# Performance work log

Measured on AMD Instinct MI355X. Metric: run time of the kernel, lower is better.

The kernel has to match this reference:

```python
import jax, jax.numpy as jnp
import numpy as np

N = 16384
F_IN = 64
F_OUT = 64


def setup_inputs() -> dict:
    key = jax.random.key(0)
    k1, k2, k3 = jax.random.split(key, 3)
    x = jax.random.normal(k1, (N, F_IN), dtype=jnp.float32)
    # dense binary adjacency (what dense_to_sparse consumes)
    adj = jax.random.randint(k2, (N, N), 0, 2).astype(jnp.float32)
    W = jax.random.normal(k3, (F_IN, F_OUT), dtype=jnp.float32) * (1.0 / np.sqrt(F_IN))
    b = jnp.zeros((F_OUT,), dtype=jnp.float32)
    return {"x": x, "adj": adj, "W": W, "b": b}


def reference(x, adj, W, b):
    # GCNConv with edge_weight from dense_to_sparse(adj), add_self_loops=True,
    # symmetric normalization: out = D^{-1/2} A_hat^T D^{-1/2} (x W) + b,
    # where A_hat = adj + I and D is the column-degree of A_hat.
    # Dropout is identity in eval mode (training=False). Activation = relu.
    deg = adj.sum(axis=0) + 1.0                      # [N] col sums incl. self-loop
    dinv = jnp.where(deg > 0, jax.lax.rsqrt(deg), 0.0)
    xw = x @ W                                       # [N, F_OUT]
    z = dinv[:, None] * xw                           # scale by source deg^-1/2
    # A_hat^T @ z = adj^T @ z + z (self-loop term), avoids materializing A + I
    out = dinv[:, None] * (adj.T @ z + z) + b
    return jax.nn.relu(out)
```

## Files before the change

kernel.cpp:

```cpp
#include <hip/hip_runtime.h>
#include <cstdint>
#include <cstddef>

#define GN 16384
#define GF 64
#define NW (GN / 32)

typedef __bf16 bf16x8 __attribute__((ext_vector_type(8)));
typedef float f32x4 __attribute__((ext_vector_type(4)));
typedef unsigned int u32x4 __attribute__((ext_vector_type(4)));

__device__ __forceinline__ bf16x8 decode8(unsigned int b) {
  unsigned int t = (b & 0xffu) * 0x8001u;
  u32x4 r;
  r[0] = (t & 0x00010001u) * 0x3F80u;
  r[1] = ((t >> 2) & 0x00010001u) * 0x3F80u;
  r[2] = ((t >> 4) & 0x00010001u) * 0x3F80u;
  r[3] = ((t >> 6) & 0x00010001u) * 0x3F80u;
  return __builtin_bit_cast(bf16x8, r);
}

__device__ __forceinline__ unsigned short f2bf(float v) {
  unsigned int u = __builtin_bit_cast(unsigned int, v);
  u += 0x7fffu + ((u >> 16) & 1u);
  return (unsigned short)(u >> 16);
}

__device__ __forceinline__ float bf2f(unsigned short s) {
  return __builtin_bit_cast(float, (unsigned int)s << 16);
}

__global__ __launch_bounds__(256) void k_pack(const float* __restrict__ adj,
                                              float* __restrict__ deg,
                                              unsigned int* __restrict__ packed) {
  const int cb = blockIdx.x >> 5;
  const int jb = blockIdx.x & 31;
  const int col0 = cb * 1024 + threadIdx.x * 4;
  const int j0 = jb * 512;
  int cnt0 = 0, cnt1 = 0, cnt2 = 0, cnt3 = 0;

  u32x4 vv0[4], vv1[4], vv2[4], vv3[4];

#pragma unroll
  for (int seg = 0; seg < 4; ++seg) {
#pragma unroll
    for (int q = 0; q < 4; ++q) {
      unsigned int w0 = 0, w1 = 0, w2 = 0, w3 = 0;
      const float* base = adj + (size_t)(j0 + seg * 128 + q * 32) * GN + col0;
#pragma unroll 8
      for (int b = 0; b < 32; ++b) {
        f32x4 a = *(const f32x4*)(base + (size_t)b * GN);
        unsigned int m = 1u << b;
        if (a.x != 0.f) w0 |= m;
        if (a.y != 0.f) w1 |= m;
        if (a.z != 0.f) w2 |= m;
        if (a.w != 0.f) w3 |= m;
      }
      vv0[seg][q] = w0; vv1[seg][q] = w1; vv2[seg][q] = w2; vv3[seg][q] = w3;
      cnt0 += __popc(w0); cnt1 += __popc(w1); cnt2 += __popc(w2); cnt3 += __popc(w3);
    }
  }
  unsigned int* p0 = packed + (size_t)(col0 + 0) * NW + (size_t)jb * 16;
  unsigned int* p1 = packed + (size_t)(col0 + 1) * NW + (size_t)jb * 16;
  unsigned int* p2 = packed + (size_t)(col0 + 2) * NW + (size_t)jb * 16;
  unsigned int* p3 = packed + (size_t)(col0 + 3) * NW + (size_t)jb * 16;
#pragma unroll
  for (int seg = 0; seg < 4; ++seg) *(u32x4*)(p0 + seg * 4) = vv0[seg];
#pragma unroll
  for (int seg = 0; seg < 4; ++seg) *(u32x4*)(p1 + seg * 4) = vv1[seg];
#pragma unroll
  for (int seg = 0; seg < 4; ++seg) *(u32x4*)(p2 + seg * 4) = vv2[seg];
#pragma unroll
  for (int seg = 0; seg < 4; ++seg) *(u32x4*)(p3 + seg * 4) = vv3[seg];

  atomicAdd(&deg[col0 + 0], (float)cnt0);
  atomicAdd(&deg[col0 + 1], (float)cnt1);
  atomicAdd(&deg[col0 + 2], (float)cnt2);
  atomicAdd(&deg[col0 + 3], (float)cnt3);
}

__global__ __launch_bounds__(256) void k_z(const float* __restrict__ x,
                                           const float* __restrict__ W,
                                           const float* __restrict__ deg,
                                           float* __restrict__ dinv,
                                           unsigned short* __restrict__ z_rm,
                                           unsigned short* __restrict__ z2) {
  __shared__ float Wl[64][64];
  __shared__ float xl[64][64];
  const int tid = threadIdx.x;
  const int f = tid & 63;
  const int w = tid >> 6;
  const int rowB = blockIdx.x * 64;

  for (int idx = tid; idx < 4096; idx += 256) {
    Wl[idx >> 6][idx & 63] = W[idx];
    xl[idx >> 6][idx & 63] = x[(size_t)rowB * 64 + idx];
  }
  __syncthreads();

  float acc[16];
#pragma unroll
  for (int r = 0; r < 16; ++r) acc[r] = 0.f;
  for (int k = 0; k < 64; ++k) {
    float wk = Wl[k][f];
#pragma unroll
    for (int r = 0; r < 16; ++r) acc[r] = fmaf(xl[w * 16 + r][k], wk, acc[r]);
  }

  const int row0 = rowB + w * 16;
  if (f < 16) {
    int row = row0 + f;
    dinv[row] = 1.0f / sqrtf(deg[row] + 1.0f);
  }

  unsigned short zs[16];
#pragma unroll
  for (int r = 0; r < 16; ++r) {
    int row = row0 + r;
    float di = 1.0f / sqrtf(deg[row] + 1.0f);
    unsigned short zb = f2bf(di * acc[r]);
    zs[r] = zb;
    z_rm[(size_t)row * GF + f] = zb;
  }
  unsigned int p[8];
#pragma unroll
  for (int i = 0; i < 8; ++i)
    p[i] = (unsigned int)zs[2 * i] | ((unsigned int)zs[2 * i + 1] << 16);
  char* dst = (char*)z2 + (size_t)((rowB >> 5) + (w >> 1)) * 4096 + f * 64 + (w & 1) * 32;
  u32x4 lo = {p[0], p[1], p[2], p[3]};
  u32x4 hi = {p[4], p[5], p[6], p[7]};
  *(u32x4*)dst = lo;
  *(u32x4*)(dst + 16) = hi;
}

__global__ __launch_bounds__(512) void k_spmm(const unsigned int* __restrict__ packed,
                                              const unsigned short* __restrict__ z2,
                                              const unsigned short* __restrict__ z_rm,
                                              const float* __restrict__ dinv,
                                              const float* __restrict__ bias,
                                              float* __restrict__ out) {
  __shared__ float red[4][64][64];
  const int i0 = blockIdx.x * 64;
  const int tid = threadIdx.x;
  const int wid = tid >> 6, lane = tid & 63;
  const int lrow = lane & 15, kb = lane >> 4;
  const int sh = kb * 8;

  f32x4 acc[4][4];
#pragma unroll
  for (int m = 0; m < 4; ++m)
#pragma unroll
    for (int n = 0; n < 4; ++n) acc[m][n] = (f32x4){0.f, 0.f, 0.f, 0.f};

  const unsigned int* pr0 = packed + (size_t)(i0 + 0 * 16 + lrow) * NW + wid * 64;
  const unsigned int* pr1 = packed + (size_t)(i0 + 1 * 16 + lrow) * NW + wid * 64;
  const unsigned int* pr2 = packed + (size_t)(i0 + 2 * 16 + lrow) * NW + wid * 64;
  const unsigned int* pr3 = packed + (size_t)(i0 + 3 * 16 + lrow) * NW + wid * 64;
  const char* zbase = (const char*)z2 + (size_t)(wid * 64) * 4096 + lrow * 64 + kb * 16;

  bf16x8 cur0 = *(const bf16x8*)(zbase + 0 * 1024);
  bf16x8 cur1 = *(const bf16x8*)(zbase + 1 * 1024);
  bf16x8 cur2 = *(const bf16x8*)(zbase + 2 * 1024);
  bf16x8 cur3 = *(const bf16x8*)(zbase + 3 * 1024);
  u32x4 bits0 = *(const u32x4*)pr0;
  u32x4 bits1 = *(const u32x4*)pr1;
  u32x4 bits2 = *(const u32x4*)pr2;
  u32x4 bits3 = *(const u32x4*)pr3;

  for (int it = 0; it < 16; ++it) {
    u32x4 nb0 = *(const u32x4*)(pr0 + 4);
    u32x4 nb1 = *(const u32x4*)(pr1 + 4);
    u32x4 nb2 = *(const u32x4*)(pr2 + 4);
    u32x4 nb3 = *(const u32x4*)(pr3 + 4);
#pragma unroll
    for (int s = 0; s < 4; ++s) {
      const char* zn = zbase + (s + 1) * 4096;
      bf16x8 n0 = *(const bf16x8*)(zn + 0 * 1024);
      bf16x8 n1 = *(const bf16x8*)(zn + 1 * 1024);
      bf16x8 n2 = *(const bf16x8*)(zn + 2 * 1024);
      bf16x8 n3 = *(const bf16x8*)(zn + 3 * 1024);

      bf16x8 a0 = decode8(bits0[s] >> sh);
      acc[0][0] = __builtin_amdgcn_mfma_f32_16x16x32_bf16(a0, cur0, acc[0][0], 0, 0, 0);
      acc[0][1] = __builtin_amdgcn_mfma_f32_16x16x32_bf16(a0, cur1, acc[0][1], 0, 0, 0);
      acc[0][2] = __builtin_amdgcn_mfma_f32_16x16x32_bf16(a0, cur2, acc[0][2], 0, 0, 0);
      acc[0][3] = __builtin_amdgcn_mfma_f32_16x16x32_bf16(a0, cur3, acc[0][3], 0, 0, 0);
      bf16x8 a1 = decode8(bits1[s] >> sh);
      acc[1][0] = __builtin_amdgcn_mfma_f32_16x16x32_bf16(a1, cur0, acc[1][0], 0, 0, 0);
      acc[1][1] = __builtin_amdgcn_mfma_f32_16x16x32_bf16(a1, cur1, acc[1][1], 0, 0, 0);
      acc[1][2] = __builtin_amdgcn_mfma_f32_16x16x32_bf16(a1, cur2, acc[1][2], 0, 0, 0);
      acc[1][3] = __builtin_amdgcn_mfma_f32_16x16x32_bf16(a1, cur3, acc[1][3], 0, 0, 0);
      bf16x8 a2 = decode8(bits2[s] >> sh);
      acc[2][0] = __builtin_amdgcn_mfma_f32_16x16x32_bf16(a2, cur0, acc[2][0], 0, 0, 0);
      acc[2][1] = __builtin_amdgcn_mfma_f32_16x16x32_bf16(a2, cur1, acc[2][1], 0, 0, 0);
      acc[2][2] = __builtin_amdgcn_mfma_f32_16x16x32_bf16(a2, cur2, acc[2][2], 0, 0, 0);
      acc[2][3] = __builtin_amdgcn_mfma_f32_16x16x32_bf16(a2, cur3, acc[2][3], 0, 0, 0);
      bf16x8 a3 = decode8(bits3[s] >> sh);
      acc[3][0] = __builtin_amdgcn_mfma_f32_16x16x32_bf16(a3, cur0, acc[3][0], 0, 0, 0);
      acc[3][1] = __builtin_amdgcn_mfma_f32_16x16x32_bf16(a3, cur1, acc[3][1], 0, 0, 0);
      acc[3][2] = __builtin_amdgcn_mfma_f32_16x16x32_bf16(a3, cur2, acc[3][2], 0, 0, 0);
      acc[3][3] = __builtin_amdgcn_mfma_f32_16x16x32_bf16(a3, cur3, acc[3][3], 0, 0, 0);

      cur0 = n0; cur1 = n1; cur2 = n2; cur3 = n3;
    }
    bits0 = nb0; bits1 = nb1; bits2 = nb2; bits3 = nb3;
    pr0 += 4; pr1 += 4; pr2 += 4; pr3 += 4;
    zbase += 16384;
  }

  if (wid < 4) {
#pragma unroll
    for (int m = 0; m < 4; ++m)
#pragma unroll
      for (int n = 0; n < 4; ++n)
#pragma unroll
        for (int r = 0; r < 4; ++r)
          red[wid][m * 16 + kb * 4 + r][n * 16 + lrow] = acc[m][n][r];
  }
  __syncthreads();
  if (wid >= 4) {
#pragma unroll
    for (int m = 0; m < 4; ++m)
#pragma unroll
      for (int n = 0; n < 4; ++n)
#pragma unroll
        for (int r = 0; r < 4; ++r)
          red[wid - 4][m * 16 + kb * 4 + r][n * 16 + lrow] += acc[m][n][r];
  }
  __syncthreads();

  const int c = tid & 63;
  const int rg = tid >> 6;
  const float bc = bias[c];
#pragma unroll
  for (int rr = 0; rr < 8; ++rr) {
    int r = rg * 8 + rr;
    int i = i0 + r;
    float s = red[0][r][c] + red[1][r][c] + red[2][r][c] + red[3][r][c];
    float o = dinv[i] * (s + bf2f(z_rm[(size_t)i * GF + c])) + bc;
    out[(size_t)i * GF + c] = fmaxf(o, 0.f);
  }
}

extern "C" void kernel_launch(void* const* d_in, const int* in_sizes, int n_in,
                              void* d_out, int out_size, void* d_ws, size_t ws_size,
                              hipStream_t stream) {
  const float* x = (const float*)d_in[0];
  const float* adj = (const float*)d_in[1];
  const float* W = (const float*)d_in[2];
  const float* bias = (const float*)d_in[3];
  float* out = (float*)d_out;

  char* ws = (char*)d_ws;
  float* deg = (float*)ws;
  float* dinv = (float*)(ws + 65536);
  unsigned short* z_rm = (unsigned short*)(ws + 131072);
  unsigned short* z2 = (unsigned short*)(ws + 131072 + 2097152);
  unsigned int* packed = (unsigned int*)(ws + 131072 + 4194304);
  if (ws_size < 37879872u) return;

  hipMemsetAsync(deg, 0, GN * sizeof(float), stream);
  k_pack<<<dim3(512), dim3(256), 0, stream>>>(adj, deg, packed);
  k_z<<<dim3(GN / 64), dim3(256), 0, stream>>>(x, W, deg, dinv, z_rm, z2);
  k_spmm<<<dim3(GN / 64), dim3(512), 0, stream>>>(packed, z2, z_rm, dinv, bias, out);
}
```

Measured before the change: 264.8 us.

## Transpose packed adjacency bitmask layout to word-major for coalesced pack and spmm

Stores the packed adjacency bits word-major (one 32-row word index per row of length N) instead of column-major. Each pack block now reads 32 full rows and writes contiguous words, with twice as many blocks. The spmm kernel gathers words with scalar loads strided by N in place of one 16-byte vector load per row. The aim is more coalesced writes and reads in the pack pass, at the cost of more, smaller loads in spmm and more atomic degree updates per block.

Result: slower. 318.1 us (+20.1%).

```diff
diff --git a/kernel.cpp b/kernel.cpp
--- a/kernel.cpp
+++ b/kernel.cpp
@@ -32,51 +32,44 @@
 
 __global__ __launch_bounds__(256) void k_pack(const float* __restrict__ adj,
                                               float* __restrict__ deg,
-                                              unsigned int* __restrict__ packed) {
-  const int cb = blockIdx.x >> 5;
-  const int jb = blockIdx.x & 31;
-  const int col0 = cb * 1024 + threadIdx.x * 4;
-  const int j0 = jb * 512;
-  int cnt0 = 0, cnt1 = 0, cnt2 = 0, cnt3 = 0;
-
-  u32x4 vv0[4], vv1[4], vv2[4], vv3[4];
-
-#pragma unroll
-  for (int seg = 0; seg < 4; ++seg) {
-#pragma unroll
-    for (int q = 0; q < 4; ++q) {
-      unsigned int w0 = 0, w1 = 0, w2 = 0, w3 = 0;
-      const float* base = adj + (size_t)(j0 + seg * 128 + q * 32) * GN + col0;
-#pragma unroll 8
-      for (int b = 0; b < 32; ++b) {
-        f32x4 a = *(const f32x4*)(base + (size_t)b * GN);
-        unsigned int m = 1u << b;
-        if (a.x != 0.f) w0 |= m;
-        if (a.y != 0.f) w1 |= m;
-        if (a.z != 0.f) w2 |= m;
-        if (a.w != 0.f) w3 |= m;
-      }
-      vv0[seg][q] = w0; vv1[seg][q] = w1; vv2[seg][q] = w2; vv3[seg][q] = w3;
-      cnt0 += __popc(w0); cnt1 += __popc(w1); cnt2 += __popc(w2); cnt3 += __popc(w3);
+                                              unsigned int* __restrict__ packedT) {
+  const int jb = (int)blockIdx.x >> 1;
+  const int ch = (int)blockIdx.x & 1;
+  const int j0 = jb * 32;
+  const int c0 = ch * 8192 + (int)threadIdx.x * 4;
+
+  unsigned int wb[8][4];
+#pragma unroll
+  for (int cc = 0; cc < 8; ++cc)
+#pragma unroll
+    for (int q = 0; q < 4; ++q) wb[cc][q] = 0;
+
+  for (int b = 0; b < 32; ++b) {
+    const float* rowp = adj + (size_t)(j0 + b) * GN + c0;
+    const unsigned int m = 1u << b;
+#pragma unroll
+    for (int cc = 0; cc < 8; ++cc) {
+      f32x4 a = *(const f32x4*)(rowp + cc * 1024);
+      if (a.x != 0.f) wb[cc][0] |= m;
+      if (a.y != 0.f) wb[cc][1] |= m;
+      if (a.z != 0.f) wb[cc][2] |= m;
+      if (a.w != 0.f) wb[cc][3] |= m;
     }
   }
-  unsigned int* p0 = packed + (size_t)(col0 + 0) * NW + (size_t)jb * 16;
-  unsigned int* p1 = packed + (size_t)(col0 + 1) * NW + (size_t)jb * 16;
-  unsigned int* p2 = packed + (size_t)(col0 + 2) * NW + (size_t)jb * 16;
-  unsigned int* p3 = packed + (size_t)(col0 + 3) * NW + (size_t)jb * 16;
-#pragma unroll
-  for (int seg = 0; seg < 4; ++seg) *(u32x4*)(p0 + seg * 4) = vv0[seg];
-#pragma unroll
-  for (int seg = 0; seg < 4; ++seg) *(u32x4*)(p1 + seg * 4) = vv1[seg];
-#pragma unroll
-  for (int seg = 0; seg < 4; ++seg) *(u32x4*)(p2 + seg * 4) = vv2[seg];
-#pragma unroll
-  for (int seg = 0; seg < 4; ++seg) *(u32x4*)(p3 + seg * 4) = vv3[seg];
-
-  atomicAdd(&deg[col0 + 0], (float)cnt0);
-  atomicAdd(&deg[col0 + 1], (float)cnt1);
-  atomicAdd(&deg[col0 + 2], (float)cnt2);
-  atomicAdd(&deg[col0 + 3], (float)cnt3);
+
+  unsigned int* dst = packedT + (size_t)jb * GN + c0;
+#pragma unroll
+  for (int cc = 0; cc < 8; ++cc) {
+    u32x4 v = {wb[cc][0], wb[cc][1], wb[cc][2], wb[cc][3]};
+    *(u32x4*)(dst + cc * 1024) = v;
+  }
+#pragma unroll
+  for (int cc = 0; cc < 8; ++cc) {
+    atomicAdd(&deg[c0 + cc * 1024 + 0], (float)__popc(wb[cc][0]));
+    atomicAdd(&deg[c0 + cc * 1024 + 1], (float)__popc(wb[cc][1]));
+    atomicAdd(&deg[c0 + cc * 1024 + 2], (float)__popc(wb[cc][2]));
+    atomicAdd(&deg[c0 + cc * 1024 + 3], (float)__popc(wb[cc][3]));
+  }
 }
 
 __global__ __launch_bounds__(256) void k_z(const float* __restrict__ x,
@@ -133,7 +126,7 @@
   *(u32x4*)(dst + 16) = hi;
 }
 
-__global__ __launch_bounds__(512) void k_spmm(const unsigned int* __restrict__ packed,
+__global__ __launch_bounds__(512) void k_spmm(const unsigned int* __restrict__ packedT,
                                               const unsigned short* __restrict__ z2,
                                               const unsigned short* __restrict__ z_rm,
                                               const float* __restrict__ dinv,
@@ -152,26 +145,34 @@
 #pragma unroll
     for (int n = 0; n < 4; ++n) acc[m][n] = (f32x4){0.f, 0.f, 0.f, 0.f};
 
-  const unsigned int* pr0 = packed + (size_t)(i0 + 0 * 16 + lrow) * NW + wid * 64;
-  const unsigned int* pr1 = packed + (size_t)(i0 + 1 * 16 + lrow) * NW + wid * 64;
-  const unsigned int* pr2 = packed + (size_t)(i0 + 2 * 16 + lrow) * NW + wid * 64;
-  const unsigned int* pr3 = packed + (size_t)(i0 + 3 * 16 + lrow) * NW + wid * 64;
+  const unsigned int* pw = packedT + (size_t)(wid * 64) * GN + i0 + lrow;
   const char* zbase = (const char*)z2 + (size_t)(wid * 64) * 4096 + lrow * 64 + kb * 16;
 
   bf16x8 cur0 = *(const bf16x8*)(zbase + 0 * 1024);
   bf16x8 cur1 = *(const bf16x8*)(zbase + 1 * 1024);
   bf16x8 cur2 = *(const bf16x8*)(zbase + 2 * 1024);
   bf16x8 cur3 = *(const bf16x8*)(zbase + 3 * 1024);
-  u32x4 bits0 = *(const u32x4*)pr0;
-  u32x4 bits1 = *(const u32x4*)pr1;
-  u32x4 bits2 = *(const u32x4*)pr2;
-  u32x4 bits3 = *(const u32x4*)pr3;
+  u32x4 bits0, bits1, bits2, bits3;
+#pragma unroll
+  for (int s = 0; s < 4; ++s) {
+    const unsigned int* ps = pw + (size_t)s * GN;
+    bits0[s] = ps[0];
+    bits1[s] = ps[16];
+    bits2[s] = ps[32];
+    bits3[s] = ps[48];
+  }
+  const unsigned int* pnext = pw + (size_t)4 * GN;
 
   for (int it = 0; it < 16; ++it) {
-    u32x4 nb0 = *(const u32x4*)(pr0 + 4);
-    u32x4 nb1 = *(const u32x4*)(pr1 + 4);
-    u32x4 nb2 = *(const u32x4*)(pr2 + 4);
-    u32x4 nb3 = *(const u32x4*)(pr3 + 4);
+    u32x4 nb0, nb1, nb2, nb3;
+#pragma unroll
+    for (int s = 0; s < 4; ++s) {
+      const unsigned int* ps = pnext + (size_t)s * GN;
+      nb0[s] = ps[0];
+      nb1[s] = ps[16];
+      nb2[s] = ps[32];
+      nb3[s] = ps[48];
+    }
 #pragma unroll
     for (int s = 0; s < 4; ++s) {
       const char* zn = zbase + (s + 1) * 4096;
@@ -204,7 +205,7 @@
       cur0 = n0; cur1 = n1; cur2 = n2; cur3 = n3;
     }
     bits0 = nb0; bits1 = nb1; bits2 = nb2; bits3 = nb3;
-    pr0 += 4; pr1 += 4; pr2 += 4; pr3 += 4;
+    pnext += (size_t)4 * GN;
     zbase += 16384;
   }
 
@@ -256,11 +257,11 @@
   float* dinv = (float*)(ws + 65536);
   unsigned short* z_rm = (unsigned short*)(ws + 131072);
   unsigned short* z2 = (unsigned short*)(ws + 131072 + 2097152);
-  unsigned int* packed = (unsigned int*)(ws + 131072 + 4194304);
-  if (ws_size < 37879872u) return;
+  unsigned int* packedT = (unsigned int*)(ws + 131072 + 4194304);
+  if (ws_size < 38141952u) return;
 
   hipMemsetAsync(deg, 0, GN * sizeof(float), stream);
-  k_pack<<<dim3(512), dim3(256), 0, stream>>>(adj, deg, packed);
+  k_pack<<<dim3(1024), dim3(256), 0, stream>>>(adj, deg, packedT);
   k_z<<<dim3(GN / 64), dim3(256), 0, stream>>>(x, W, deg, dinv, z_rm, z2);
-  k_spmm<<<dim3(GN / 64), dim3(512), 0, stream>>>(packed, z2, z_rm, dinv, bias, out);
-}
+  k_spmm<<<dim3(GN / 64), dim3(512), 0, stream>>>(packedT, z2, z_rm, dinv, bias, out);
+}
```
